# Kernel tuning notes

Hardware: AMD Instinct MI355X
Metric: run time of the kernel (lower is better)

Reference implementation:

```python
import jax, jax.numpy as jnp
import numpy as np

EMBED = 1024
HEADS = 16
HEAD_DIM = EMBED // HEADS
B, S = 2, 2048


def setup_inputs() -> dict:
    key = jax.random.key(0)
    ks = jax.random.split(key, 11)
    sc = 1.0 / np.sqrt(EMBED)
    d = {
        'query': jax.random.normal(ks[0], (B, S, EMBED), jnp.float32),
        'key':   jax.random.normal(ks[1], (B, S, EMBED), jnp.float32),
        'value': jax.random.normal(ks[2], (B, S, EMBED), jnp.float32),
        'Wq': jax.random.normal(ks[3], (EMBED, EMBED), jnp.float32) * sc,
        'bq': jnp.zeros((EMBED,), jnp.float32),
        'Wk': jax.random.normal(ks[4], (EMBED, EMBED), jnp.float32) * sc,
        'bk': jnp.zeros((EMBED,), jnp.float32),
        'Wv': jax.random.normal(ks[5], (EMBED, EMBED), jnp.float32) * sc,
        'bv': jnp.zeros((EMBED,), jnp.float32),
        'Wo': jax.random.normal(ks[6], (EMBED, EMBED), jnp.float32) * sc,
        'bo': jnp.zeros((EMBED,), jnp.float32),
    }
    return d


def _split_heads(x):
    b, s, _ = x.shape
    return x.reshape(b, s, HEADS, HEAD_DIM).transpose(0, 2, 1, 3)  # [B,H,S,D]


def reference(query, key, value, Wq, bq, Wk, bk, Wv, bv, Wo, bo):
    # nn.Linear: y = x @ W^T + b
    q = _split_heads(query @ Wq.T + bq)
    k = _split_heads(key @ Wk.T + bk)
    v = _split_heads(value @ Wv.T + bv)
    scale = 1.0 / np.sqrt(HEAD_DIM).astype(np.float32)
    attn = jnp.einsum('bhqd,bhkd->bhqk', q, k) * scale  # [B,H,S,S]
    attn = jax.nn.softmax(attn, axis=-1)
    out = jnp.einsum('bhqk,bhkd->bhqd', attn, v)
    out = out.transpose(0, 2, 1, 3).reshape(query.shape[0], -1, EMBED)
    return out @ Wo.T + bo
```

## Files before the change

### kernel.cpp

```cpp
#include <hip/hip_runtime.h>

typedef _Float16 f16;
typedef __fp16   fp16n2 __attribute__((ext_vector_type(2)));
typedef _Float16 f16x8 __attribute__((ext_vector_type(8)));
typedef float    f32x2 __attribute__((ext_vector_type(2)));
typedef float    f32x4 __attribute__((ext_vector_type(4)));
typedef float    f32x16 __attribute__((ext_vector_type(16)));
typedef int      i32x2 __attribute__((ext_vector_type(2)));
typedef unsigned short u16;
typedef unsigned long long u64;

#define B_ 2
#define S_ 2048
#define E_ 1024
#define H_ 16
#define D_ 64
#define M_ (B_*S_)
#define LOG2E 1.44269504088896340736f

__device__ __forceinline__ f32x4 mfma16(f16x8 a, f16x8 b, f32x4 c) {
  return __builtin_amdgcn_mfma_f32_16x16x32_f16(a, b, c, 0, 0, 0);
}
__device__ __forceinline__ f32x16 mfma32(f16x8 a, f16x8 b, f32x16 c) {
  return __builtin_amdgcn_mfma_f32_32x32x16_f16(a, b, c, 0, 0, 0);
}

__device__ __forceinline__ void gload_lds16(const void* g, void* l) {
  __builtin_amdgcn_global_load_lds(
      (const __attribute__((address_space(1))) unsigned int*)g,
      (__attribute__((address_space(3))) unsigned int*)l, 16, 0, 0);
}

__device__ __forceinline__ int pkrtz(float a, float b) {
  union { fp16n2 h; int i; } u;
  u.h = __builtin_amdgcn_cvt_pkrtz(a, b);
  return u.i;
}

__device__ __forceinline__ u16 f16bits(float x) {
  union { f16 h; u16 u; } c; c.h = (f16)x; return c.u;
}

__device__ __forceinline__ f32x16 Z16() {
  f32x16 z = {0.f,0.f,0.f,0.f,0.f,0.f,0.f,0.f,0.f,0.f,0.f,0.f,0.f,0.f,0.f,0.f};
  return z;
}

__device__ __forceinline__ f32x2 pr2(const f32x16& v, int j) {
  return (f32x2){v[2 * j], v[2 * j + 1]};
}

__global__ __launch_bounds__(256) void cast_all(
    const float* __restrict__ q, const float* __restrict__ k, const float* __restrict__ v,
    const float* __restrict__ wq, const float* __restrict__ wk,
    const float* __restrict__ wv, const float* __restrict__ wo,
    f16* __restrict__ xq, f16* __restrict__ xk, f16* __restrict__ xv,
    f16* __restrict__ wqh, f16* __restrict__ wkh, f16* __restrict__ wvh,
    f16* __restrict__ woh) {
  int i = blockIdx.x * 256 + threadIdx.x;
  const float* src; f16* dst; int off;
  if (i < 3 * 524288) {
    int seg = i >> 19; off = i & 524287;
    src = seg == 0 ? q : seg == 1 ? k : v;
    dst = seg == 0 ? xq : seg == 1 ? xk : xv;
  } else {
    int j = i - 3 * 524288;
    int seg = j >> 17; off = j & 131071;
    src = seg == 0 ? wq : seg == 1 ? wk : seg == 2 ? wv : wo;
    dst = seg == 0 ? wqh : seg == 1 ? wkh : seg == 2 ? wvh : woh;
  }
  const float4* s = (const float4*)src;
  float4 a = s[off * 2], b = s[off * 2 + 1];
  f16x8 o = { (f16)a.x, (f16)a.y, (f16)a.z, (f16)a.w,
              (f16)b.x, (f16)b.y, (f16)b.z, (f16)b.w };
  *(f16x8*)&dst[(size_t)off * 8] = o;
}

__device__ __forceinline__ void gemm_core(const f16* __restrict__ A,
                                          const f16* __restrict__ Bm,
                                          f32x4 (&acc)[4][4]) {
  __shared__ f16 Al[2][128 * 32];
  __shared__ f16 Bl[2][128 * 32];
  const int tid = threadIdx.x;
  const int w = tid >> 6, lane = tid & 63, lg = lane >> 4, ll = lane & 15;
  const int m0 = blockIdx.x * 128, n0 = blockIdx.y * 128;
  const int wr = (w >> 1) * 64, wc = (w & 1) * 64;

  const f32x4 zero4 = {0.f, 0.f, 0.f, 0.f};
#pragma unroll
  for (int m = 0; m < 4; ++m)
#pragma unroll
    for (int n = 0; n < 4; ++n) acc[m][n] = zero4;

  for (int k0 = 0; k0 < 1024; k0 += 64) {
    __syncthreads();
#pragma unroll
    for (int ks = 0; ks < 2; ++ks)
#pragma unroll
      for (int it = 0; it < 2; ++it) {
        int chunk = it * 256 + w * 64 + lane;
        int row = chunk >> 2;
        int c8  = (chunk & 3) * 8;
        gload_lds16(&A [(size_t)(m0 + row) * 1024 + k0 + ks * 32 + c8],
                    &Al[ks][(it * 256 + w * 64) * 8]);
        gload_lds16(&Bm[(size_t)(n0 + row) * 1024 + k0 + ks * 32 + c8],
                    &Bl[ks][(it * 256 + w * 64) * 8]);
      }
    __syncthreads();

#pragma unroll
    for (int ks = 0; ks < 2; ++ks) {
      f16x8 af[4], bf[4];
#pragma unroll
      for (int m = 0; m < 4; ++m) af[m] = *(const f16x8*)&Al[ks][(wr + m * 16 + ll) * 32 + lg * 8];
#pragma unroll
      for (int n = 0; n < 4; ++n) bf[n] = *(const f16x8*)&Bl[ks][(wc + n * 16 + ll) * 32 + lg * 8];
#pragma unroll
      for (int m = 0; m < 4; ++m)
#pragma unroll
        for (int n = 0; n < 4; ++n) acc[m][n] = mfma16(af[m], bf[n], acc[m][n]);
    }
  }
}

__global__ __launch_bounds__(256) void gemm_qkv(
    const f16* __restrict__ Xq, const f16* __restrict__ Xk, const f16* __restrict__ Xv,
    const f16* __restrict__ Wq, const f16* __restrict__ Wk, const f16* __restrict__ Wv,
    const float* __restrict__ bq, const float* __restrict__ bk, const float* __restrict__ bv,
    f16* __restrict__ Qb, f16* __restrict__ Kb, f16* __restrict__ Vt) {
  const int z = blockIdx.z;
  const f16*   A    = (z == 0) ? Xq : (z == 1) ? Xk : Xv;
  const f16*   Bm   = (z == 0) ? Wq : (z == 1) ? Wk : Wv;
  const float* bias = (z == 0) ? bq : (z == 1) ? bk : bv;
  const float scale = (z == 0) ? (0.125f * LOG2E) : 1.0f;

  f32x4 acc[4][4];
  gemm_core(A, Bm, acc);

  const int tid = threadIdx.x;
  const int w = tid >> 6, lane = tid & 63, lg = lane >> 4, ll = lane & 15;
  const int m0 = blockIdx.x * 128, n0 = blockIdx.y * 128;
  const int wr = (w >> 1) * 64, wc = (w & 1) * 64;

  if (z == 2) {
#pragma unroll
    for (int m = 0; m < 4; ++m)
#pragma unroll
      for (int n = 0; n < 4; ++n) {
        int col = n0 + wc + n * 16 + ll;
        float bv_ = bias[col];
        int h = col >> 6, d = col & 63;
        int rowb = m0 + wr + m * 16 + lg * 4;
        int b = rowb >> 11, s = rowb & 2047;
        u64 pk = (u64)f16bits(acc[m][n][0] + bv_)
               | ((u64)f16bits(acc[m][n][1] + bv_) << 16)
               | ((u64)f16bits(acc[m][n][2] + bv_) << 32)
               | ((u64)f16bits(acc[m][n][3] + bv_) << 48);
        *(u64*)&Vt[(((size_t)(b * H_ + h)) * D_ + d) * S_ + s] = pk;
      }
    return;
  }

  f16* dst = (z == 0) ? Qb : Kb;
#pragma unroll
  for (int m = 0; m < 4; ++m)
#pragma unroll
    for (int n = 0; n < 4; ++n) {
      int col = n0 + wc + n * 16 + ll;
      float bv_ = bias[col];
      int h = col >> 6, d = col & 63;
#pragma unroll
      for (int r = 0; r < 4; ++r) {
        int row = m0 + wr + m * 16 + lg * 4 + r;
        int b = row >> 11, s = row & 2047;
        float v = (acc[m][n][r] + bv_) * scale;
        dst[(((size_t)(b * H_ + h)) * S_ + s) * D_ + d] = (f16)v;
      }
    }
}

__global__ __launch_bounds__(256) void gemm_out(const f16* __restrict__ A,
                                                const f16* __restrict__ W,
                                                const float* __restrict__ bias,
                                                float* __restrict__ out) {
  f32x4 acc[4][4];
  gemm_core(A, W, acc);
  const int tid = threadIdx.x;
  const int w = tid >> 6, lane = tid & 63, lg = lane >> 4, ll = lane & 15;
  const int m0 = blockIdx.x * 128, n0 = blockIdx.y * 128;
  const int wr = (w >> 1) * 64, wc = (w & 1) * 64;
#pragma unroll
  for (int m = 0; m < 4; ++m)
#pragma unroll
    for (int n = 0; n < 4; ++n) {
      int col = n0 + wc + n * 16 + ll;
      float bv_ = bias[col];
#pragma unroll
      for (int r = 0; r < 4; ++r) {
        int row = m0 + wr + m * 16 + lg * 4 + r;
        out[(size_t)row * 1024 + col] = acc[m][n][r] + bv_;
      }
    }
}

__global__ __launch_bounds__(512, 4) void attn_fwd(const f16* __restrict__ Q,
                                                   const f16* __restrict__ K,
                                                   const f16* __restrict__ VT,
                                                   f16* __restrict__ O) {
  const int qt = blockIdx.x, bh = blockIdx.y;
  const int tid = threadIdx.x;
  const int w = tid >> 6, lane = tid & 63;
  const int ql = lane & 31, hi = lane >> 5;
  const int qsub = w & 3, kvh = w >> 2;

  __shared__ __align__(16) char smem[65536];
  char* hbase = smem + kvh * 32768;

  const f16* Qb = Q  + (size_t)bh * S_ * D_;
  const f16* Kb = K  + (size_t)bh * S_ * D_ + (size_t)(kvh * 1024) * D_;
  const f16* Vb = VT + (size_t)bh * D_ * S_ + kvh * 1024;
  const int q0 = qt * 128 + qsub * 32;

  f16x8 qf[4];
#pragma unroll
  for (int ks = 0; ks < 4; ++ks)
    qf[ks] = *(const f16x8*)&Qb[(size_t)(q0 + ql) * 64 + ks * 16 + hi * 8];

  f32x16 accO[2];
  accO[0] = Z16(); accO[1] = Z16();
  float m_r = -1e30f, l_r = 0.f;

  const int seg = w & 3;
  const int lr = lane >> 3;
  const int lc = lane & 7;
  const int cs = lc ^ lr;

#define STAGE(kt_)                                                             \
  {                                                                            \
    char* Kl_ = hbase + ((kt_) & 1) * 16384;                                   \
    char* Vl_ = Kl_ + 8192;                                                    \
    _Pragma("unroll")                                                          \
    for (int i_ = 0; i_ < 2; ++i_) {                                           \
      int r_ = seg * 16 + i_ * 8 + lr;                         \
      gload_lds16(&Kb[(size_t)((kt_) * 64 + r_) * 64 + cs * 8],                \
                  Kl_ + seg * 2048 + i_ * 1024);                               \
      gload_lds16(&Vb[(size_t)r_ * S_ + (kt_) * 64 + cs * 8],                  \
                  Vl_ + seg * 2048 + i_ * 1024);                               \
    }                                                                          \
  }

  STAGE(0);

#pragma unroll 1
  for (int kt = 0; kt < 16; ++kt) {
    __syncthreads();
    if (kt + 1 < 16) STAGE(kt + 1);

    char* KlB = hbase + (kt & 1) * 16384;
    char* VlB = KlB + 8192;

    f32x16 accS[2];
    __builtin_amdgcn_s_setprio(1);
#pragma unroll
    for (int c = 0; c < 2; ++c) {
      int row = c * 32 + ql;
      int rb = row * 128, sw = (row & 7) << 4;
      f16x8 kf0 = *(const f16x8*)(KlB + rb + ((hi * 16) ^ sw));
      accS[c] = mfma32(kf0, qf[0], Z16());
#pragma unroll
      for (int ks = 1; ks < 4; ++ks) {
        f16x8 kf = *(const f16x8*)(KlB + rb + (((ks * 2 + hi) * 16) ^ sw));
        accS[c] = mfma32(kf, qf[ks], accS[c]);
      }
    }
    __builtin_amdgcn_s_setprio(0);

    f32x2 mj[8];
#pragma unroll
    for (int j = 0; j < 8; ++j)
      mj[j] = __builtin_elementwise_max(pr2(accS[0], j), pr2(accS[1], j));
#pragma unroll
    for (int j = 0; j < 4; ++j)
      mj[j] = __builtin_elementwise_max(mj[j], mj[j + 4]);
    mj[0] = __builtin_elementwise_max(mj[0], mj[2]);
    mj[1] = __builtin_elementwise_max(mj[1], mj[3]);
    mj[0] = __builtin_elementwise_max(mj[0], mj[1]);
    float t = fmaxf(mj[0].x, mj[0].y);
    t = fmaxf(t, __shfl_xor(t, 32));

    if (__any(t > m_r + 8.0f)) {
      float mnew = fmaxf(m_r, t);
      float alpha = __builtin_amdgcn_exp2f(m_r - mnew);
      l_r *= alpha;
      accO[0] = accO[0] * alpha;
      accO[1] = accO[1] * alpha;
      m_r = mnew;
    }
    const f32x2 mb = {m_r, m_r};
    f32x2 rs2 = {0.f, 0.f};
#pragma unroll
    for (int c = 0; c < 2; ++c)
#pragma unroll
      for (int j = 0; j < 8; ++j) {
        f32x2 xp = pr2(accS[c], j) - mb;
        float p0 = __builtin_amdgcn_exp2f(xp.x);
        float p1 = __builtin_amdgcn_exp2f(xp.y);
        accS[c][2 * j]     = p0;
        accS[c][2 * j + 1] = p1;
        rs2 += (f32x2){p0, p1};
      }
    float rs = rs2.x + rs2.y;
    rs += __shfl_xor(rs, 32);
    l_r += rs;

#pragma unroll
    for (int c = 0; c < 2; ++c)
#pragma unroll
      for (int s = 0; s < 2; ++s) {
        int b0 = s * 8;
        int a0 = pkrtz(accS[c][b0 + 0], accS[c][b0 + 1]);
        int a1 = pkrtz(accS[c][b0 + 2], accS[c][b0 + 3]);
        int a2 = pkrtz(accS[c][b0 + 4], accS[c][b0 + 5]);
        int a3 = pkrtz(accS[c][b0 + 6], accS[c][b0 + 7]);
        i32x2 r02 = __builtin_amdgcn_permlane32_swap(a0, a2, false, false);
        i32x2 r13 = __builtin_amdgcn_permlane32_swap(a1, a3, false, false);
        union { int i[4]; f16x8 h; } pf;
        pf.i[0] = r02.x; pf.i[1] = r13.x; pf.i[2] = r02.y; pf.i[3] = r13.y;
        int kvb = c * 64 + s * 32 + hi * 16;
        __builtin_amdgcn_s_setprio(1);
#pragma unroll
        for (int dc = 0; dc < 2; ++dc) {
          int dr = dc * 32 + ql;
          f16x8 vf = *(const f16x8*)(VlB + dr * 128 + (kvb ^ ((dr & 7) << 4)));
          accO[dc] = mfma32(vf, pf.h, accO[dc]);
        }
        __builtin_amdgcn_s_setprio(0);
      }
  }
#undef STAGE

  __syncthreads();
  float* mlB = (float*)smem;
  if (kvh == 1) {
    if (hi == 0) {
      mlB[qsub * 64 + ql * 2]     = m_r;
      mlB[qsub * 64 + ql * 2 + 1] = l_r;
    }
#pragma unroll
    for (int dc = 0; dc < 2; ++dc)
#pragma unroll
      for (int g = 0; g < 4; ++g) {
        int d0 = g * 8 + hi * 4 + dc * 32;
        f32x4 v = { accO[dc][g * 4 + 0], accO[dc][g * 4 + 1],
                    accO[dc][g * 4 + 2], accO[dc][g * 4 + 3] };
        *(f32x4*)(smem + 32768 + qsub * 8192 + ql * 256 + ((d0 * 4) ^ ((ql & 7) << 4))) = v;
      }
  }
  __syncthreads();
  f16* Ep = (f16*)(smem + 1024);
  if (kvh == 0) {
    float m2 = mlB[qsub * 64 + ql * 2], l2 = mlB[qsub * 64 + ql * 2 + 1];
    float mm = fmaxf(m_r, m2);
    float a1 = __builtin_amdgcn_exp2f(m_r - mm), a2 = __builtin_amdgcn_exp2f(m2 - mm);
    float inv = 1.0f / (l_r * a1 + l2 * a2);
    a1 *= inv; a2 *= inv;
#pragma unroll
    for (int dc = 0; dc < 2; ++dc)
#pragma unroll
      for (int g = 0; g < 4; ++g) {
        int d0 = g * 8 + hi * 4 + dc * 32;
        f32x4 o2 = *(const f32x4*)(smem + 32768 + qsub * 8192 + ql * 256 +
                                   ((d0 * 4) ^ ((ql & 7) << 4)));
        u64 pk = (u64)f16bits(accO[dc][g * 4 + 0] * a1 + o2[0] * a2)
               | ((u64)f16bits(accO[dc][g * 4 + 1] * a1 + o2[1] * a2) << 16)
               | ((u64)f16bits(accO[dc][g * 4 + 2] * a1 + o2[2] * a2) << 32)
               | ((u64)f16bits(accO[dc][g * 4 + 3] * a1 + o2[3] * a2) << 48);
        *(u64*)&Ep[(qsub * 32 + ql) * 68 + d0] = pk;
      }
  }
  __syncthreads();
  const int b = bh >> 4, h = bh & 15;
#pragma unroll
  for (int pass = 0; pass < 2; ++pass) {
    int idx = pass * 512 + tid;
    int row = idx >> 3, cx = idx & 7;
    f16x8 v = *(const f16x8*)&Ep[row * 68 + cx * 8];
    *(f16x8*)&O[((size_t)(b * S_ + qt * 128 + row)) * E_ + h * 64 + cx * 8] = v;
  }
}

extern "C" void kernel_launch(void* const* d_in, const int* in_sizes, int n_in,
                              void* d_out, int out_size, void* d_ws, size_t ws_size,
                              hipStream_t stream) {
  (void)in_sizes; (void)n_in; (void)out_size; (void)ws_size;
  const float* q  = (const float*)d_in[0];
  const float* k  = (const float*)d_in[1];
  const float* v  = (const float*)d_in[2];
  const float* Wq = (const float*)d_in[3];
  const float* bq = (const float*)d_in[4];
  const float* Wk = (const float*)d_in[5];
  const float* bk = (const float*)d_in[6];
  const float* Wv = (const float*)d_in[7];
  const float* bv = (const float*)d_in[8];
  const float* Wo = (const float*)d_in[9];
  const float* bo = (const float*)d_in[10];
  float* out = (float*)d_out;

  f16* ws  = (f16*)d_ws;
  f16* Xq  = ws;
  f16* Xk  = Xq  + (size_t)M_ * E_;
  f16* Xv  = Xk  + (size_t)M_ * E_;
  f16* Wqh = Xv  + (size_t)M_ * E_;
  f16* Wkh = Wqh + (size_t)E_ * E_;
  f16* Wvh = Wkh + (size_t)E_ * E_;
  f16* Woh = Wvh + (size_t)E_ * E_;
  f16* Qb  = Woh + (size_t)E_ * E_;
  f16* Kb  = Qb  + (size_t)M_ * E_;
  f16* VTb = Kb  + (size_t)M_ * E_;
  f16* AO  = Xq;

  cast_all<<<8192, 256, 0, stream>>>(q, k, v, Wq, Wk, Wv, Wo,
                                     Xq, Xk, Xv, Wqh, Wkh, Wvh, Woh);

  gemm_qkv<<<dim3(M_ / 128, E_ / 128, 3), 256, 0, stream>>>(
      Xq, Xk, Xv, Wqh, Wkh, Wvh, bq, bk, bv, Qb, Kb, VTb);

  attn_fwd<<<dim3(S_ / 128, B_ * H_), 512, 0, stream>>>(Qb, Kb, VTb, AO);

  gemm_out<<<dim3(M_ / 128, E_ / 128), 256, 0, stream>>>(AO, Woh, bo, out);
}
```

Before: 138.1 us.

## Remap GEMM block indices per XCD and halve output GEMM tile width

The QKV projection now uses a flat 1D grid whose block index is remapped so that blocks sharing an XCD (block index mod 8) work on the same weight column groups, aiming to improve L2 reuse of the weights on MI355X's chiplet layout. The output projection gets its own 128x64 tile kernel, which doubles its block count to 512 to fill more CUs, and uses the same XCD-aware remap. Narrower tiles lower arithmetic intensity and mean the A tiles are reloaded more often.

```diff
diff --git a/kernel.cpp b/kernel.cpp
--- a/kernel.cpp
+++ b/kernel.cpp
@@ -78,12 +78,12 @@
 
 __device__ __forceinline__ void gemm_core(const f16* __restrict__ A,
                                           const f16* __restrict__ Bm,
+                                          int m0, int n0,
                                           f32x4 (&acc)[4][4]) {
   __shared__ f16 Al[2][128 * 32];
   __shared__ f16 Bl[2][128 * 32];
   const int tid = threadIdx.x;
   const int w = tid >> 6, lane = tid & 63, lg = lane >> 4, ll = lane & 15;
-  const int m0 = blockIdx.x * 128, n0 = blockIdx.y * 128;
   const int wr = (w >> 1) * 64, wc = (w & 1) * 64;
 
   const f32x4 zero4 = {0.f, 0.f, 0.f, 0.f};
@@ -128,18 +128,25 @@
     const f16* __restrict__ Wq, const f16* __restrict__ Wk, const f16* __restrict__ Wv,
     const float* __restrict__ bq, const float* __restrict__ bk, const float* __restrict__ bv,
     f16* __restrict__ Qb, f16* __restrict__ Kb, f16* __restrict__ Vt) {
-  const int z = blockIdx.z;
+  const int n_ = blockIdx.x;
+  const int xcd = n_ & 7;
+  const int k_  = n_ >> 3;
+  const int x   = k_ & 31;
+  const int cg  = xcd * 3 + (k_ >> 5);
+  const int y   = cg & 7;
+  const int z   = cg >> 3;
+
   const f16*   A    = (z == 0) ? Xq : (z == 1) ? Xk : Xv;
   const f16*   Bm   = (z == 0) ? Wq : (z == 1) ? Wk : Wv;
   const float* bias = (z == 0) ? bq : (z == 1) ? bk : bv;
   const float scale = (z == 0) ? (0.125f * LOG2E) : 1.0f;
+  const int m0 = x * 128, n0 = y * 128;
 
   f32x4 acc[4][4];
-  gemm_core(A, Bm, acc);
+  gemm_core(A, Bm, m0, n0, acc);
 
   const int tid = threadIdx.x;
   const int w = tid >> 6, lane = tid & 63, lg = lane >> 4, ll = lane & 15;
-  const int m0 = blockIdx.x * 128, n0 = blockIdx.y * 128;
   const int wr = (w >> 1) * 64, wc = (w & 1) * 64;
 
   if (z == 2) {
@@ -183,16 +190,62 @@
                                                 const f16* __restrict__ W,
                                                 const float* __restrict__ bias,
                                                 float* __restrict__ out) {
-  f32x4 acc[4][4];
-  gemm_core(A, W, acc);
+  const int n_ = blockIdx.x;
+  const int xcd = n_ & 7;
+  const int k_  = n_ >> 3;
+  const int x   = k_ & 31;
+  const int y   = xcd * 2 + (k_ >> 5);
+  const int m0 = x * 128, n0 = y * 64;
+
+  __shared__ f16 Al[2][128 * 32];
+  __shared__ f16 Bl[2][64 * 32];
   const int tid = threadIdx.x;
   const int w = tid >> 6, lane = tid & 63, lg = lane >> 4, ll = lane & 15;
-  const int m0 = blockIdx.x * 128, n0 = blockIdx.y * 128;
-  const int wr = (w >> 1) * 64, wc = (w & 1) * 64;
+  const int wr = (w >> 1) * 64, wc = (w & 1) * 32;
+
+  f32x4 acc[4][2];
+  const f32x4 zero4 = {0.f, 0.f, 0.f, 0.f};
+#pragma unroll
+  for (int m = 0; m < 4; ++m) { acc[m][0] = zero4; acc[m][1] = zero4; }
+
+  for (int k0 = 0; k0 < 1024; k0 += 64) {
+    __syncthreads();
+#pragma unroll
+    for (int ks = 0; ks < 2; ++ks) {
+#pragma unroll
+      for (int it = 0; it < 2; ++it) {
+        int chunk = it * 256 + tid;
+        int row = chunk >> 2, c8 = (chunk & 3) * 8;
+        gload_lds16(&A[(size_t)(m0 + row) * 1024 + k0 + ks * 32 + c8],
+                    &Al[ks][chunk * 8]);
+      }
+      {
+        int chunk = tid;
+        int row = chunk >> 2, c8 = (chunk & 3) * 8;
+        gload_lds16(&W[(size_t)(n0 + row) * 1024 + k0 + ks * 32 + c8],
+                    &Bl[ks][chunk * 8]);
+      }
+    }
+    __syncthreads();
+
+#pragma unroll
+    for (int ks = 0; ks < 2; ++ks) {
+      f16x8 af[4], bf[2];
+#pragma unroll
+      for (int m = 0; m < 4; ++m) af[m] = *(const f16x8*)&Al[ks][(wr + m * 16 + ll) * 32 + lg * 8];
+#pragma unroll
+      for (int n = 0; n < 2; ++n) bf[n] = *(const f16x8*)&Bl[ks][(wc + n * 16 + ll) * 32 + lg * 8];
+#pragma unroll
+      for (int m = 0; m < 4; ++m)
+#pragma unroll
+        for (int n = 0; n < 2; ++n) acc[m][n] = mfma16(af[m], bf[n], acc[m][n]);
+    }
+  }
+
 #pragma unroll
   for (int m = 0; m < 4; ++m)
 #pragma unroll
-    for (int n = 0; n < 4; ++n) {
+    for (int n = 0; n < 2; ++n) {
       int col = n0 + wc + n * 16 + ll;
       float bv_ = bias[col];
 #pragma unroll
@@ -241,7 +294,7 @@
     char* Vl_ = Kl_ + 8192;                                                    \
     _Pragma("unroll")                                                          \
     for (int i_ = 0; i_ < 2; ++i_) {                                           \
-      int r_ = seg * 16 + i_ * 8 + lr;                         \
+      int r_ = seg * 16 + i_ * 8 + lr;                                         \
       gload_lds16(&Kb[(size_t)((kt_) * 64 + r_) * 64 + cs * 8],                \
                   Kl_ + seg * 2048 + i_ * 1024);                               \
       gload_lds16(&Vb[(size_t)r_ * S_ + (kt_) * 64 + cs * 8],                  \
@@ -422,10 +475,10 @@
   cast_all<<<8192, 256, 0, stream>>>(q, k, v, Wq, Wk, Wv, Wo,
                                      Xq, Xk, Xv, Wqh, Wkh, Wvh, Woh);
 
-  gemm_qkv<<<dim3(M_ / 128, E_ / 128, 3), 256, 0, stream>>>(
+  gemm_qkv<<<768, 256, 0, stream>>>(
       Xq, Xk, Xv, Wqh, Wkh, Wvh, bq, bk, bv, Qb, Kb, VTb);
 
   attn_fwd<<<dim3(S_ / 128, B_ * H_), 512, 0, stream>>>(Qb, Kb, VTb, AO);
 
-  gemm_out<<<dim3(M_ / 128, E_ / 128), 256, 0, stream>>>(AO, Woh, bo, out);
-}
+  gemm_out<<<512, 256, 0, stream>>>(AO, Woh, bo, out);
+}
```

Result: no change. 136.1 us (-1.4%).
